# Performance work log

Measured on AMD Instinct MI355X. Metric: run time of the kernel, lower is better.

## Reference

```python
import jax, jax.numpy as jnp
import numpy as np

NODELEN = 394
N_NODES = 50000
N_EDGES = 200000
IN_DIM = 2 * NODELEN  # 788
H2 = 192
EMB = 128


def setup_inputs() -> dict:
    key = jax.random.key(0)
    ks = jax.random.split(key, 12)
    inp = {
        'features': jax.random.normal(ks[0], (N_NODES, NODELEN), dtype=jnp.float32),
        'src': jax.random.randint(ks[1], (N_EDGES,), 0, N_NODES),
        'dst': jax.random.randint(ks[2], (N_EDGES,), 0, N_NODES),
        # AutoEncoder params (Linear weights stored as [in, out])
        'W_enc1': jax.random.normal(ks[3], (IN_DIM, H2), dtype=jnp.float32) / np.sqrt(IN_DIM),
        'b_enc1': jnp.zeros((H2,), dtype=jnp.float32),
        'W_enc3': jax.random.normal(ks[4], (H2, EMB), dtype=jnp.float32) / np.sqrt(H2),
        'b_enc3': jnp.zeros((EMB,), dtype=jnp.float32),
        'W_dec1': jax.random.normal(ks[5], (EMB, H2), dtype=jnp.float32) / np.sqrt(EMB),
        'b_dec1': jnp.zeros((H2,), dtype=jnp.float32),
        'W_dec3': jax.random.normal(ks[6], (H2, IN_DIM), dtype=jnp.float32) / np.sqrt(H2),
        'b_dec3': jnp.zeros((IN_DIM,), dtype=jnp.float32),
    }
    return inp


def _segment_mean(msgs, dst, inv_deg, n):
    # msgs: [E, F] gathered neighbor features; mean over incoming edges per node
    return jax.ops.segment_sum(msgs, dst, num_segments=n) * inv_deg


def reference(features, src, dst, W_enc1, b_enc1, W_enc3, b_enc3,
              W_dec1, b_dec1, W_dec3, b_dec3):
    n = features.shape[0]
    ones = jnp.ones(src.shape[0], dtype=features.dtype)
    deg = jax.ops.segment_sum(ones, dst, num_segments=n)
    # nodes with no neighbors fall back to the zero dummy vector (as in source)
    inv_deg = (1.0 / jnp.maximum(deg, 1.0))[:, None]

    # depth-1 aggregation: mean of raw neighbor features, then feat[0] := 0
    h1 = _segment_mean(features[src], dst, inv_deg, n)
    h1 = h1.at[:, 0].set(0.0)
    # depth-2 aggregation: mean of depth-1 aggregates of neighbors, feat[0] := 0
    h2 = _segment_mean(h1[src], dst, inv_deg, n)
    h2 = h2.at[:, 0].set(0.0)

    # concatenated embedding with positions 0 and NODELEN zeroed
    emb = jnp.concatenate([features, h2], axis=1)  # [N, 788]
    emb = emb.at[:, 0].set(0.0).at[:, NODELEN].set(0.0)

    # AutoEncoder forward (dropout is identity at inference)
    x = jax.nn.relu(emb @ W_enc1 + b_enc1)
    encoded = x @ W_enc3 + b_enc3
    y = jax.nn.relu(encoded @ W_dec1 + b_dec1)
    decoded = y @ W_dec3 + b_dec3
    return encoded, decoded, emb
```

## Files before the change

### kernel.cpp

```cpp
#include <hip/hip_runtime.h>
#include <hip/hip_bf16.h>

#define NODELEN 394
#define IN_DIM 788
#define H2DIM 192
#define EMBDIM 128
#define NCHUNK 197

typedef __attribute__((ext_vector_type(4))) float f32x4;
typedef __attribute__((ext_vector_type(8))) short bfrag;

static __device__ __forceinline__ unsigned short f2bf(float f) {
    union { float f; unsigned u; } v; v.f = f;
    unsigned r = v.u + 0x7FFFu + ((v.u >> 16) & 1u);
    return (unsigned short)(r >> 16);
}
static __device__ __forceinline__ float bf2f(unsigned short h) {
    union { unsigned u; float f; } v; v.u = ((unsigned)h) << 16;
    return v.f;
}


__global__ void count_deg(const int* __restrict__ dst, int* __restrict__ deg, int e) {
    int i = blockIdx.x * blockDim.x + threadIdx.x;
    if (i < e) atomicAdd(&deg[dst[i]], 1);
}

__global__ void block_sum(const int* __restrict__ deg, int* __restrict__ bsum, int n) {
    __shared__ int s[256];
    int t = threadIdx.x;
    int i = blockIdx.x * 256 + t;
    s[t] = (i < n) ? deg[i] : 0;
    __syncthreads();
    for (int d = 128; d > 0; d >>= 1) {
        if (t < d) s[t] += s[t + d];
        __syncthreads();
    }
    if (t == 0) bsum[blockIdx.x] = s[0];
}

__global__ void scan_bsums(int* bsum, int nb) {
    __shared__ int s[256];
    int t = threadIdx.x;
    int x0 = (t < nb) ? bsum[t] : 0;
    s[t] = x0;
    __syncthreads();
    for (int d = 1; d < 256; d <<= 1) {
        int u = (t >= d) ? s[t - d] : 0;
        __syncthreads();
        s[t] += u;
        __syncthreads();
    }
    if (t < nb) bsum[t] = s[t] - x0;
}

__global__ void block_scan(const int* __restrict__ deg, const int* __restrict__ boff,
                           int* __restrict__ rowstart, int* __restrict__ cursor,
                           float* __restrict__ inv, int n) {
    __shared__ int s[256];
    int t = threadIdx.x;
    int i = blockIdx.x * 256 + t;
    int x0 = (i < n) ? deg[i] : 0;
    s[t] = x0;
    __syncthreads();
    for (int d = 1; d < 256; d <<= 1) {
        int u = (t >= d) ? s[t - d] : 0;
        __syncthreads();
        s[t] += u;
        __syncthreads();
    }
    if (i < n) {
        int r = boff[blockIdx.x] + s[t] - x0;
        rowstart[i] = r;
        cursor[i] = r;
        inv[i] = 1.0f / fmaxf((float)x0, 1.0f);
    }
}

__global__ void fill_edges(const int* __restrict__ src, const int* __restrict__ dst,
                           int* __restrict__ cursor, int* __restrict__ elist, int e) {
    int i = blockIdx.x * blockDim.x + threadIdx.x;
    if (i < e) {
        int p = atomicAdd(&cursor[dst[i]], 1);
        elist[p] = src[i];
    }
}


__global__ __launch_bounds__(256) void gather1(
        const float* __restrict__ feat, const int* __restrict__ rowstart,
        const int* __restrict__ deg, const float* __restrict__ inv,
        const int* __restrict__ elist, unsigned short* __restrict__ h1) {
    const int node = blockIdx.x;
    const int c = threadIdx.x;
    if (c >= NCHUNK) return;
    const int beg = rowstart[node];
    const int dc = deg[node];
    const float s = inv[node];
    const size_t off = (size_t)c * 2;

    float ax = 0.f, ay = 0.f, bx = 0.f, by = 0.f;
    float cx = 0.f, cy = 0.f, dx = 0.f, dy = 0.f;
    int j = 0;
    for (; j + 3 < dc; j += 4) {
        int n0 = elist[beg + j], n1 = elist[beg + j + 1];
        int n2 = elist[beg + j + 2], n3 = elist[beg + j + 3];
        float2 v0 = *(const float2*)(feat + (size_t)n0 * NODELEN + off);
        float2 v1 = *(const float2*)(feat + (size_t)n1 * NODELEN + off);
        float2 v2 = *(const float2*)(feat + (size_t)n2 * NODELEN + off);
        float2 v3 = *(const float2*)(feat + (size_t)n3 * NODELEN + off);
        ax += v0.x; ay += v0.y; bx += v1.x; by += v1.y;
        cx += v2.x; cy += v2.y; dx += v3.x; dy += v3.y;
    }
    for (; j < dc; ++j) {
        int n0 = elist[beg + j];
        float2 v0 = *(const float2*)(feat + (size_t)n0 * NODELEN + off);
        ax += v0.x; ay += v0.y;
    }
    float fx = (ax + bx + cx + dx) * s;
    float fy = (ay + by + cy + dy) * s;
    if (c == 0) fx = 0.f;
    unsigned out = ((unsigned)f2bf(fy) << 16) | (unsigned)f2bf(fx);
    *(unsigned*)(h1 + (size_t)node * NODELEN + off) = out;
}

__global__ __launch_bounds__(256) void gather2_emb(
        const float* __restrict__ feat, const unsigned* __restrict__ h1,
        const int* __restrict__ rowstart, const int* __restrict__ deg,
        const float* __restrict__ inv, const int* __restrict__ elist,
        float* __restrict__ emb, unsigned* __restrict__ emb16) {
    const int node = blockIdx.x;
    const int c = threadIdx.x;
    if (c >= NCHUNK) {
        if (emb16 && c >= NCHUNK && c < NCHUNK + 3) {
            int p = 394 + (c - NCHUNK) * 2;
            emb16[(size_t)node * 400 + p] = 0u;
            emb16[(size_t)node * 400 + p + 1] = 0u;
        }
        return;
    }
    const int beg = rowstart[node];
    const int dc = deg[node];
    const float s = inv[node];

    float ax = 0.f, ay = 0.f, bx = 0.f, by = 0.f;
    float cx = 0.f, cy = 0.f, dx = 0.f, dy = 0.f;
    int j = 0;
    for (; j + 3 < dc; j += 4) {
        int n0 = elist[beg + j], n1 = elist[beg + j + 1];
        int n2 = elist[beg + j + 2], n3 = elist[beg + j + 3];
        unsigned u0 = h1[(size_t)n0 * NCHUNK + c];
        unsigned u1 = h1[(size_t)n1 * NCHUNK + c];
        unsigned u2 = h1[(size_t)n2 * NCHUNK + c];
        unsigned u3 = h1[(size_t)n3 * NCHUNK + c];
        ax += bf2f((unsigned short)u0); ay += bf2f((unsigned short)(u0 >> 16));
        bx += bf2f((unsigned short)u1); by += bf2f((unsigned short)(u1 >> 16));
        cx += bf2f((unsigned short)u2); cy += bf2f((unsigned short)(u2 >> 16));
        dx += bf2f((unsigned short)u3); dy += bf2f((unsigned short)(u3 >> 16));
    }
    for (; j < dc; ++j) {
        int n0 = elist[beg + j];
        unsigned u0 = h1[(size_t)n0 * NCHUNK + c];
        ax += bf2f((unsigned short)u0); ay += bf2f((unsigned short)(u0 >> 16));
    }
    float hx = (ax + bx + cx + dx) * s;
    float hy = (ay + by + cy + dy) * s;

    const float* fr = feat + (size_t)node * NODELEN;
    float* er = emb + (size_t)node * IN_DIM;
    float2 fv = *(const float2*)(fr + c * 2);
    if (c == 0) { fv.x = 0.f; hx = 0.f; }
    *(float2*)(er + c * 2) = fv;
    float2 hv; hv.x = hx; hv.y = hy;
    *(float2*)(er + NODELEN + c * 2) = hv;

    if (emb16) {
        unsigned* e16 = emb16 + (size_t)node * 400;
        e16[c]          = ((unsigned)f2bf(fv.y) << 16) | (unsigned)f2bf(fv.x);
        e16[NCHUNK + c] = ((unsigned)f2bf(hy)  << 16) | (unsigned)f2bf(hx);
    }
}

__device__ __forceinline__ void tr_one(const float* W, unsigned short* Wt,
                                       int K, int N, int Kp, int idx) {
    int nrow = idx / Kp, k = idx - nrow * Kp;
    Wt[idx] = (k < K) ? f2bf(W[(size_t)k * N + nrow]) : (unsigned short)0;
}

#define T1E (192 * 800)
#define T2E (128 * 192)
#define T3E (192 * 128)
#define T4E (788 * 192)

__global__ void transpose_all(const float* __restrict__ W1, unsigned short* __restrict__ Wt1,
                              const float* __restrict__ W2, unsigned short* __restrict__ Wt2,
                              const float* __restrict__ W3, unsigned short* __restrict__ Wt3,
                              const float* __restrict__ W4, unsigned short* __restrict__ Wt4) {
    int idx = blockIdx.x * 256 + threadIdx.x;
    if (idx < T1E) { tr_one(W1, Wt1, IN_DIM, H2DIM, 800, idx); return; }
    idx -= T1E;
    if (idx < T2E) { tr_one(W2, Wt2, H2DIM, EMBDIM, 192, idx); return; }
    idx -= T2E;
    if (idx < T3E) { tr_one(W3, Wt3, EMBDIM, H2DIM, 128, idx); return; }
    idx -= T3E;
    if (idx < T4E) { tr_one(W4, Wt4, H2DIM, IN_DIM, 192, idx); return; }
}

template <int MF, int NF, int RELU, int A_F32, int OUTF, int OUTB>
__global__ __launch_bounds__(256) void gemm_mfma(
    const void* __restrict__ Aptr, const unsigned short* __restrict__ Wt,
    const float* __restrict__ bias, float* __restrict__ Cf,
    unsigned short* __restrict__ Cb, int M, int N, int K, int lda, int Ksteps)
{
    constexpr int BMr = 32 * MF;
    constexpr int BNr = 32 * NF;
    __shared__ unsigned short As[BMr][40];
    __shared__ unsigned short Bs[BNr][40];

    const int tid = threadIdx.x;
    const int wid = tid >> 6, l = tid & 63;
    const int wm = wid >> 1, wn = wid & 1;
    const int lr = l & 15, lk = l >> 4;
    const int m0 = blockIdx.x * BMr;
    const int n0 = blockIdx.y * BNr;
    const int Kp = Ksteps * 32;

    f32x4 acc[MF][NF];
    #pragma unroll
    for (int i = 0; i < MF; ++i)
        #pragma unroll
        for (int j = 0; j < NF; ++j)
            acc[i][j] = (f32x4){0.f, 0.f, 0.f, 0.f};

    float bv[NF];
    #pragma unroll
    for (int j = 0; j < NF; ++j) {
        int gn = n0 + wn * NF * 16 + j * 16 + lr;
        bv[j] = (gn < N) ? bias[gn] : 0.f;
    }

    for (int kt = 0; kt < Ksteps; ++kt) {
        int k0 = kt * 32;
        if (A_F32) {
            const float* A = (const float*)Aptr;
            for (int a = tid; a < BMr * 4; a += 256) {
                int row = a >> 2, q = a & 3;
                int gm = m0 + row, gk = k0 + q * 8;
                float4 v0 = make_float4(0.f, 0.f, 0.f, 0.f);
                float4 v1 = make_float4(0.f, 0.f, 0.f, 0.f);
                if (gm < M) {
                    if (gk < K)     v0 = *(const float4*)(A + (size_t)gm * lda + gk);
                    if (gk + 4 < K) v1 = *(const float4*)(A + (size_t)gm * lda + gk + 4);
                }
                union { unsigned short u[8]; bfrag v; } pk;
                pk.u[0] = f2bf(v0.x); pk.u[1] = f2bf(v0.y);
                pk.u[2] = f2bf(v0.z); pk.u[3] = f2bf(v0.w);
                pk.u[4] = f2bf(v1.x); pk.u[5] = f2bf(v1.y);
                pk.u[6] = f2bf(v1.z); pk.u[7] = f2bf(v1.w);
                *(bfrag*)&As[row][q * 8] = pk.v;
            }
        } else {
            const unsigned short* A = (const unsigned short*)Aptr;
            for (int a = tid; a < BMr * 2; a += 256) {
                int row = a >> 1, h = a & 1;
                int gm = m0 + row;
                bfrag v0 = {0,0,0,0,0,0,0,0}, v1 = {0,0,0,0,0,0,0,0};
                if (gm < M) {
                    const unsigned short* p = A + (size_t)gm * lda + k0 + h * 16;
                    v0 = *(const bfrag*)p;
                    v1 = *(const bfrag*)(p + 8);
                }
                *(bfrag*)&As[row][h * 16]     = v0;
                *(bfrag*)&As[row][h * 16 + 8] = v1;
            }
        }
        for (int a = tid; a < BNr * 2; a += 256) {
            int row = a >> 1, h = a & 1;
            int gn = n0 + row;
            bfrag v0 = {0,0,0,0,0,0,0,0}, v1 = {0,0,0,0,0,0,0,0};
            if (gn < N) {
                const unsigned short* p = Wt + (size_t)gn * Kp + k0 + h * 16;
                v0 = *(const bfrag*)p;
                v1 = *(const bfrag*)(p + 8);
            }
            *(bfrag*)&Bs[row][h * 16]     = v0;
            *(bfrag*)&Bs[row][h * 16 + 8] = v1;
        }
        __syncthreads();

        bfrag af[MF], bfr[NF];
        #pragma unroll
        for (int i = 0; i < MF; ++i)
            af[i] = *(const bfrag*)&As[wm * MF * 16 + i * 16 + lr][lk * 8];
        #pragma unroll
        for (int j = 0; j < NF; ++j)
            bfr[j] = *(const bfrag*)&Bs[wn * NF * 16 + j * 16 + lr][lk * 8];
        #pragma unroll
        for (int i = 0; i < MF; ++i)
            #pragma unroll
            for (int j = 0; j < NF; ++j)
                acc[i][j] = __builtin_amdgcn_mfma_f32_16x16x32_bf16(af[i], bfr[j], acc[i][j], 0, 0, 0);
        __syncthreads();
    }

    #pragma unroll
    for (int i = 0; i < MF; ++i) {
        #pragma unroll
        for (int j = 0; j < NF; ++j) {
            #pragma unroll
            for (int r = 0; r < 4; ++r) {
                int gm = m0 + wm * MF * 16 + i * 16 + lk * 4 + r;
                int gn = n0 + wn * NF * 16 + j * 16 + lr;
                if (gm < M && gn < N) {
                    float v = acc[i][j][r] + bv[j];
                    if (RELU) v = fmaxf(v, 0.f);
                    if (OUTF) Cf[(size_t)gm * N + gn] = v;
                    if (OUTB) Cb[(size_t)gm * N + gn] = f2bf(v);
                }
            }
        }
    }
}


extern "C" void kernel_launch(void* const* d_in, const int* in_sizes, int n_in,
                              void* d_out, int out_size, void* d_ws, size_t ws_size,
                              hipStream_t stream) {
    const float* features = (const float*)d_in[0];
    const int*   src      = (const int*)d_in[1];
    const int*   dst      = (const int*)d_in[2];
    const float* W_enc1   = (const float*)d_in[3];
    const float* b_enc1   = (const float*)d_in[4];
    const float* W_enc3   = (const float*)d_in[5];
    const float* b_enc3   = (const float*)d_in[6];
    const float* W_dec1   = (const float*)d_in[7];
    const float* b_dec1   = (const float*)d_in[8];
    const float* W_dec3   = (const float*)d_in[9];
    const float* b_dec3   = (const float*)d_in[10];

    const int n = in_sizes[0] / NODELEN;
    const int e = in_sizes[1];

    float* encoded = (float*)d_out;
    float* decoded = encoded + (size_t)n * EMBDIM;
    float* emb     = decoded + (size_t)n * IN_DIM;

    char* ws = (char*)d_ws;
    const size_t NEED_A = 134000000;
    const int useA = (ws_size >= NEED_A) ? 1 : 0;

    unsigned short* emb16;
    unsigned short* h1;
    unsigned short* x16, *enc16, *y16;
    unsigned short* Wt1, *Wt2, *Wt3, *Wt4;
    float* inv; int *deg, *rowstart, *cursor, *elist, *bsum;

    if (useA) {
        emb16    = (unsigned short*)(ws + 0);
        h1       = (unsigned short*)(ws + 80000000);
        x16      = (unsigned short*)(ws + 80000000);
        enc16    = (unsigned short*)(ws + 99200000);
        y16      = (unsigned short*)(ws + 112000000);
        Wt1      = (unsigned short*)(ws + 131200000);
        Wt2      = (unsigned short*)(ws + 131600000);
        Wt3      = (unsigned short*)(ws + 131700000);
        Wt4      = (unsigned short*)(ws + 131800000);
        inv      = (float*)(ws + 132200000);
        deg      = (int*)  (ws + 132400000);
        rowstart = (int*)  (ws + 132600000);
        cursor   = (int*)  (ws + 132800000);
        elist    = (int*)  (ws + 133000000);
        bsum     = (int*)  (ws + 133800000);
    } else {
        emb16    = nullptr;
        h1       = (unsigned short*)(ws + 0);
        x16      = (unsigned short*)(ws + 0);
        enc16    = (unsigned short*)(ws + 19200000);
        y16      = (unsigned short*)(ws + 32000000);
        Wt1      = (unsigned short*)(ws + 52000000);
        Wt2      = (unsigned short*)(ws + 52400000);
        Wt3      = (unsigned short*)(ws + 52500000);
        Wt4      = (unsigned short*)(ws + 52600000);
        inv      = (float*)(ws + 53000000);
        deg      = (int*)  (ws + 53200000);
        rowstart = (int*)  (ws + 53400000);
        cursor   = (int*)  (ws + 53600000);
        elist    = (int*)  (ws + 53800000);
        bsum     = (int*)  (ws + 54600000);
    }

    const int nb = (n + 255) / 256;
    const int eb = (e + 255) / 256;

    transpose_all<<<(T1E + T2E + T3E + T4E + 255) / 256, 256, 0, stream>>>(
        W_enc1, Wt1, W_enc3, Wt2, W_dec1, Wt3, W_dec3, Wt4);

    hipMemsetAsync(deg, 0, (size_t)n * sizeof(int), stream);
    count_deg<<<eb, 256, 0, stream>>>(dst, deg, e);
    block_sum<<<nb, 256, 0, stream>>>(deg, bsum, n);
    scan_bsums<<<1, 256, 0, stream>>>(bsum, nb);
    block_scan<<<nb, 256, 0, stream>>>(deg, bsum, rowstart, cursor, inv, n);
    fill_edges<<<eb, 256, 0, stream>>>(src, dst, cursor, elist, e);

    gather1<<<n, 256, 0, stream>>>(features, rowstart, deg, inv, elist, h1);
    gather2_emb<<<n, 256, 0, stream>>>(features, (const unsigned*)h1, rowstart, deg,
                                       inv, elist, emb, (unsigned*)emb16);

    const int MB = (n + 127) / 128;
    if (useA) {
        gemm_mfma<4, 6, 1, 0, 0, 1><<<dim3(MB, 1), 256, 0, stream>>>(
            emb16, Wt1, b_enc1, nullptr, x16, n, H2DIM, 800, 800, 25);
    } else {
        gemm_mfma<4, 6, 1, 1, 0, 1><<<dim3(MB, 1), 256, 0, stream>>>(
            emb, Wt1, b_enc1, nullptr, x16, n, H2DIM, IN_DIM, IN_DIM, 25);
    }
    gemm_mfma<4, 4, 0, 0, 1, 1><<<dim3(MB, 1), 256, 0, stream>>>(
        x16, Wt2, b_enc3, encoded, enc16, n, EMBDIM, H2DIM, H2DIM, 6);
    gemm_mfma<4, 6, 1, 0, 0, 1><<<dim3(MB, 1), 256, 0, stream>>>(
        enc16, Wt3, b_dec1, nullptr, y16, n, H2DIM, EMBDIM, EMBDIM, 4);
    gemm_mfma<4, 6, 0, 0, 1, 0><<<dim3(MB, 5), 256, 0, stream>>>(
        y16, Wt4, b_dec3, decoded, nullptr, n, IN_DIM, H2DIM, H2DIM, 6);
}
```

Baseline: 420.7 us.

## Fuse four autoencoder GEMMs into one kernel keeping intermediates in LDS

Replaces the four separate MFMA GEMM launches with a single kernel that processes 64-row tiles through encoder and decoder layers, holding hidden activations in shared memory instead of writing bf16 intermediates to global memory. It also drops the bf16 emb16 copy and reads the fp32 emb directly with conversion on load. This removes intermediate global traffic and three launches. In exchange it uses smaller M tiles with more weight reloads per block, serial per-block stages, and higher LDS usage that may limit occupancy.

Measured after the change: 387.7 us. 1.09x faster.

```diff
diff --git a/kernel.cpp b/kernel.cpp
--- a/kernel.cpp
+++ b/kernel.cpp
@@ -128,17 +128,10 @@
         const float* __restrict__ feat, const unsigned* __restrict__ h1,
         const int* __restrict__ rowstart, const int* __restrict__ deg,
         const float* __restrict__ inv, const int* __restrict__ elist,
-        float* __restrict__ emb, unsigned* __restrict__ emb16) {
+        float* __restrict__ emb) {
     const int node = blockIdx.x;
     const int c = threadIdx.x;
-    if (c >= NCHUNK) {
-        if (emb16 && c >= NCHUNK && c < NCHUNK + 3) {
-            int p = 394 + (c - NCHUNK) * 2;
-            emb16[(size_t)node * 400 + p] = 0u;
-            emb16[(size_t)node * 400 + p + 1] = 0u;
-        }
-        return;
-    }
+    if (c >= NCHUNK) return;
     const int beg = rowstart[node];
     const int dc = deg[node];
     const float s = inv[node];
@@ -173,12 +166,6 @@
     *(float2*)(er + c * 2) = fv;
     float2 hv; hv.x = hx; hv.y = hy;
     *(float2*)(er + NODELEN + c * 2) = hv;
-
-    if (emb16) {
-        unsigned* e16 = emb16 + (size_t)node * 400;
-        e16[c]          = ((unsigned)f2bf(fv.y) << 16) | (unsigned)f2bf(fv.x);
-        e16[NCHUNK + c] = ((unsigned)f2bf(hy)  << 16) | (unsigned)f2bf(hx);
-    }
 }
 
 __device__ __forceinline__ void tr_one(const float* W, unsigned short* Wt,
@@ -206,51 +193,44 @@
     if (idx < T4E) { tr_one(W4, Wt4, H2DIM, IN_DIM, 192, idx); return; }
 }
 
-template <int MF, int NF, int RELU, int A_F32, int OUTF, int OUTB>
-__global__ __launch_bounds__(256) void gemm_mfma(
-    const void* __restrict__ Aptr, const unsigned short* __restrict__ Wt,
-    const float* __restrict__ bias, float* __restrict__ Cf,
-    unsigned short* __restrict__ Cb, int M, int N, int K, int lda, int Ksteps)
+__global__ __launch_bounds__(256) void mlp_fused(
+    const float* __restrict__ emb,
+    const unsigned short* __restrict__ Wt1,
+    const unsigned short* __restrict__ Wt2,
+    const unsigned short* __restrict__ Wt3,
+    const unsigned short* __restrict__ Wt4,
+    const float* __restrict__ b1, const float* __restrict__ b2,
+    const float* __restrict__ b3, const float* __restrict__ b4,
+    float* __restrict__ encoded, float* __restrict__ decoded, int M)
 {
-    constexpr int BMr = 32 * MF;
-    constexpr int BNr = 32 * NF;
-    __shared__ unsigned short As[BMr][40];
-    __shared__ unsigned short Bs[BNr][40];
+    __shared__ unsigned short As[64][40];
+    __shared__ unsigned short Bs[192][40];
+    __shared__ unsigned short XY[64][200];
+    __shared__ unsigned short EN[64][136];
 
     const int tid = threadIdx.x;
     const int wid = tid >> 6, l = tid & 63;
     const int wm = wid >> 1, wn = wid & 1;
     const int lr = l & 15, lk = l >> 4;
-    const int m0 = blockIdx.x * BMr;
-    const int n0 = blockIdx.y * BNr;
-    const int Kp = Ksteps * 32;
-
-    f32x4 acc[MF][NF];
-    #pragma unroll
-    for (int i = 0; i < MF; ++i)
-        #pragma unroll
-        for (int j = 0; j < NF; ++j)
-            acc[i][j] = (f32x4){0.f, 0.f, 0.f, 0.f};
-
-    float bv[NF];
-    #pragma unroll
-    for (int j = 0; j < NF; ++j) {
-        int gn = n0 + wn * NF * 16 + j * 16 + lr;
-        bv[j] = (gn < N) ? bias[gn] : 0.f;
-    }
-
-    for (int kt = 0; kt < Ksteps; ++kt) {
-        int k0 = kt * 32;
-        if (A_F32) {
-            const float* A = (const float*)Aptr;
-            for (int a = tid; a < BMr * 4; a += 256) {
-                int row = a >> 2, q = a & 3;
+    const int m0 = blockIdx.x * 64;
+
+    {
+        f32x4 acc[2][6];
+        #pragma unroll
+        for (int i = 0; i < 2; ++i)
+            #pragma unroll
+            for (int j = 0; j < 6; ++j) acc[i][j] = (f32x4){0.f, 0.f, 0.f, 0.f};
+
+        for (int kt = 0; kt < 25; ++kt) {
+            const int k0 = kt * 32;
+            {
+                int row = tid >> 2, q = tid & 3;
                 int gm = m0 + row, gk = k0 + q * 8;
                 float4 v0 = make_float4(0.f, 0.f, 0.f, 0.f);
                 float4 v1 = make_float4(0.f, 0.f, 0.f, 0.f);
                 if (gm < M) {
-                    if (gk < K)     v0 = *(const float4*)(A + (size_t)gm * lda + gk);
-                    if (gk + 4 < K) v1 = *(const float4*)(A + (size_t)gm * lda + gk + 4);
+                    if (gk < IN_DIM)     v0 = *(const float4*)(emb + (size_t)gm * IN_DIM + gk);
+                    if (gk + 4 < IN_DIM) v1 = *(const float4*)(emb + (size_t)gm * IN_DIM + gk + 4);
                 }
                 union { unsigned short u[8]; bfrag v; } pk;
                 pk.u[0] = f2bf(v0.x); pk.u[1] = f2bf(v0.y);
@@ -259,66 +239,184 @@
                 pk.u[6] = f2bf(v1.z); pk.u[7] = f2bf(v1.w);
                 *(bfrag*)&As[row][q * 8] = pk.v;
             }
-        } else {
-            const unsigned short* A = (const unsigned short*)Aptr;
-            for (int a = tid; a < BMr * 2; a += 256) {
+            for (int a = tid; a < 384; a += 256) {
                 int row = a >> 1, h = a & 1;
-                int gm = m0 + row;
+                const unsigned short* p = Wt1 + (size_t)row * 800 + k0 + h * 16;
+                *(bfrag*)&Bs[row][h * 16]     = *(const bfrag*)p;
+                *(bfrag*)&Bs[row][h * 16 + 8] = *(const bfrag*)(p + 8);
+            }
+            __syncthreads();
+            bfrag af[2], bf[6];
+            #pragma unroll
+            for (int i = 0; i < 2; ++i) af[i] = *(const bfrag*)&As[wm * 32 + i * 16 + lr][lk * 8];
+            #pragma unroll
+            for (int j = 0; j < 6; ++j) bf[j] = *(const bfrag*)&Bs[wn * 96 + j * 16 + lr][lk * 8];
+            #pragma unroll
+            for (int i = 0; i < 2; ++i)
+                #pragma unroll
+                for (int j = 0; j < 6; ++j)
+                    acc[i][j] = __builtin_amdgcn_mfma_f32_16x16x32_bf16(af[i], bf[j], acc[i][j], 0, 0, 0);
+            __syncthreads();
+        }
+        float bv[6];
+        #pragma unroll
+        for (int j = 0; j < 6; ++j) bv[j] = b1[wn * 96 + j * 16 + lr];
+        #pragma unroll
+        for (int i = 0; i < 2; ++i)
+            #pragma unroll
+            for (int j = 0; j < 6; ++j)
+                #pragma unroll
+                for (int r = 0; r < 4; ++r) {
+                    int m = wm * 32 + i * 16 + lk * 4 + r;
+                    int n1 = wn * 96 + j * 16 + lr;
+                    XY[m][n1] = f2bf(fmaxf(acc[i][j][r] + bv[j], 0.f));
+                }
+        __syncthreads();
+    }
+
+    {
+        f32x4 acc[2][4];
+        #pragma unroll
+        for (int i = 0; i < 2; ++i)
+            #pragma unroll
+            for (int j = 0; j < 4; ++j) acc[i][j] = (f32x4){0.f, 0.f, 0.f, 0.f};
+
+        for (int kt = 0; kt < 6; ++kt) {
+            const int k0 = kt * 32;
+            {
+                int row = tid >> 1, h = tid & 1;
+                const unsigned short* p = Wt2 + (size_t)row * 192 + k0 + h * 16;
+                *(bfrag*)&Bs[row][h * 16]     = *(const bfrag*)p;
+                *(bfrag*)&Bs[row][h * 16 + 8] = *(const bfrag*)(p + 8);
+            }
+            __syncthreads();
+            bfrag af[2], bf[4];
+            #pragma unroll
+            for (int i = 0; i < 2; ++i) af[i] = *(const bfrag*)&XY[wm * 32 + i * 16 + lr][k0 + lk * 8];
+            #pragma unroll
+            for (int j = 0; j < 4; ++j) bf[j] = *(const bfrag*)&Bs[wn * 64 + j * 16 + lr][lk * 8];
+            #pragma unroll
+            for (int i = 0; i < 2; ++i)
+                #pragma unroll
+                for (int j = 0; j < 4; ++j)
+                    acc[i][j] = __builtin_amdgcn_mfma_f32_16x16x32_bf16(af[i], bf[j], acc[i][j], 0, 0, 0);
+            __syncthreads();
+        }
+        float bv[4];
+        #pragma unroll
+        for (int j = 0; j < 4; ++j) bv[j] = b2[wn * 64 + j * 16 + lr];
+        #pragma unroll
+        for (int i = 0; i < 2; ++i)
+            #pragma unroll
+            for (int j = 0; j < 4; ++j)
+                #pragma unroll
+                for (int r = 0; r < 4; ++r) {
+                    int m = wm * 32 + i * 16 + lk * 4 + r;
+                    int n2 = wn * 64 + j * 16 + lr;
+                    float v = acc[i][j][r] + bv[j];
+                    int gm = m0 + m;
+                    if (gm < M) encoded[(size_t)gm * EMBDIM + n2] = v;
+                    EN[m][n2] = f2bf(v);
+                }
+        __syncthreads();
+    }
+
+    {
+        f32x4 acc[2][6];
+        #pragma unroll
+        for (int i = 0; i < 2; ++i)
+            #pragma unroll
+            for (int j = 0; j < 6; ++j) acc[i][j] = (f32x4){0.f, 0.f, 0.f, 0.f};
+
+        for (int kt = 0; kt < 4; ++kt) {
+            const int k0 = kt * 32;
+            for (int a = tid; a < 384; a += 256) {
+                int row = a >> 1, h = a & 1;
+                const unsigned short* p = Wt3 + (size_t)row * 128 + k0 + h * 16;
+                *(bfrag*)&Bs[row][h * 16]     = *(const bfrag*)p;
+                *(bfrag*)&Bs[row][h * 16 + 8] = *(const bfrag*)(p + 8);
+            }
+            __syncthreads();
+            bfrag af[2], bf[6];
+            #pragma unroll
+            for (int i = 0; i < 2; ++i) af[i] = *(const bfrag*)&EN[wm * 32 + i * 16 + lr][k0 + lk * 8];
+            #pragma unroll
+            for (int j = 0; j < 6; ++j) bf[j] = *(const bfrag*)&Bs[wn * 96 + j * 16 + lr][lk * 8];
+            #pragma unroll
+            for (int i = 0; i < 2; ++i)
+                #pragma unroll
+                for (int j = 0; j < 6; ++j)
+                    acc[i][j] = __builtin_amdgcn_mfma_f32_16x16x32_bf16(af[i], bf[j], acc[i][j], 0, 0, 0);
+            __syncthreads();
+        }
+        float bv[6];
+        #pragma unroll
+        for (int j = 0; j < 6; ++j) bv[j] = b3[wn * 96 + j * 16 + lr];
+        #pragma unroll
+        for (int i = 0; i < 2; ++i)
+            #pragma unroll
+            for (int j = 0; j < 6; ++j)
+                #pragma unroll
+                for (int r = 0; r < 4; ++r) {
+                    int m = wm * 32 + i * 16 + lk * 4 + r;
+                    int n3 = wn * 96 + j * 16 + lr;
+                    XY[m][n3] = f2bf(fmaxf(acc[i][j][r] + bv[j], 0.f));
+                }
+        __syncthreads();
+    }
+
+    for (int nc = 0; nc < 7; ++nc) {
+        f32x4 acc[2][4];
+        #pragma unroll
+        for (int i = 0; i < 2; ++i)
+            #pragma unroll
+            for (int j = 0; j < 4; ++j) acc[i][j] = (f32x4){0.f, 0.f, 0.f, 0.f};
+
+        for (int kt = 0; kt < 6; ++kt) {
+            const int k0 = kt * 32;
+            {
+                int row = tid >> 1, h = tid & 1;
+                int gn = nc * 128 + row;
                 bfrag v0 = {0,0,0,0,0,0,0,0}, v1 = {0,0,0,0,0,0,0,0};
-                if (gm < M) {
-                    const unsigned short* p = A + (size_t)gm * lda + k0 + h * 16;
+                if (gn < IN_DIM) {
+                    const unsigned short* p = Wt4 + (size_t)gn * 192 + k0 + h * 16;
                     v0 = *(const bfrag*)p;
                     v1 = *(const bfrag*)(p + 8);
                 }
-                *(bfrag*)&As[row][h * 16]     = v0;
-                *(bfrag*)&As[row][h * 16 + 8] = v1;
+                *(bfrag*)&Bs[row][h * 16]     = v0;
+                *(bfrag*)&Bs[row][h * 16 + 8] = v1;
             }
+            __syncthreads();
+            bfrag af[2], bf[4];
+            #pragma unroll
+            for (int i = 0; i < 2; ++i) af[i] = *(const bfrag*)&XY[wm * 32 + i * 16 + lr][k0 + lk * 8];
+            #pragma unroll
+            for (int j = 0; j < 4; ++j) bf[j] = *(const bfrag*)&Bs[wn * 64 + j * 16 + lr][lk * 8];
+            #pragma unroll
+            for (int i = 0; i < 2; ++i)
+                #pragma unroll
+                for (int j = 0; j < 4; ++j)
+                    acc[i][j] = __builtin_amdgcn_mfma_f32_16x16x32_bf16(af[i], bf[j], acc[i][j], 0, 0, 0);
+            __syncthreads();
         }
-        for (int a = tid; a < BNr * 2; a += 256) {
-            int row = a >> 1, h = a & 1;
-            int gn = n0 + row;
-            bfrag v0 = {0,0,0,0,0,0,0,0}, v1 = {0,0,0,0,0,0,0,0};
-            if (gn < N) {
-                const unsigned short* p = Wt + (size_t)gn * Kp + k0 + h * 16;
-                v0 = *(const bfrag*)p;
-                v1 = *(const bfrag*)(p + 8);
-            }
-            *(bfrag*)&Bs[row][h * 16]     = v0;
-            *(bfrag*)&Bs[row][h * 16 + 8] = v1;
+        float bv[4];
+        #pragma unroll
+        for (int j = 0; j < 4; ++j) {
+            int n4 = nc * 128 + wn * 64 + j * 16 + lr;
+            bv[j] = (n4 < IN_DIM) ? b4[n4] : 0.f;
         }
-        __syncthreads();
-
-        bfrag af[MF], bfr[NF];
-        #pragma unroll
-        for (int i = 0; i < MF; ++i)
-            af[i] = *(const bfrag*)&As[wm * MF * 16 + i * 16 + lr][lk * 8];
-        #pragma unroll
-        for (int j = 0; j < NF; ++j)
-            bfr[j] = *(const bfrag*)&Bs[wn * NF * 16 + j * 16 + lr][lk * 8];
-        #pragma unroll
-        for (int i = 0; i < MF; ++i)
-            #pragma unroll
-            for (int j = 0; j < NF; ++j)
-                acc[i][j] = __builtin_amdgcn_mfma_f32_16x16x32_bf16(af[i], bfr[j], acc[i][j], 0, 0, 0);
-        __syncthreads();
-    }
-
-    #pragma unroll
-    for (int i = 0; i < MF; ++i) {
-        #pragma unroll
-        for (int j = 0; j < NF; ++j) {
-            #pragma unroll
-            for (int r = 0; r < 4; ++r) {
-                int gm = m0 + wm * MF * 16 + i * 16 + lk * 4 + r;
-                int gn = n0 + wn * NF * 16 + j * 16 + lr;
-                if (gm < M && gn < N) {
-                    float v = acc[i][j][r] + bv[j];
-                    if (RELU) v = fmaxf(v, 0.f);
-                    if (OUTF) Cf[(size_t)gm * N + gn] = v;
-                    if (OUTB) Cb[(size_t)gm * N + gn] = f2bf(v);
-                }
-            }
-        }
+        #pragma unroll
+        for (int i = 0; i < 2; ++i)
+            #pragma unroll
+            for (int j = 0; j < 4; ++j)
+                #pragma unroll
+                for (int r = 0; r < 4; ++r) {
+                    int m = wm * 32 + i * 16 + lk * 4 + r;
+                    int n4 = nc * 128 + wn * 64 + j * 16 + lr;
+                    int gm = m0 + m;
+                    if (gm < M && n4 < IN_DIM)
+                        decoded[(size_t)gm * IN_DIM + n4] = acc[i][j][r] + bv[j];
+                }
     }
 }
 
@@ -346,48 +444,17 @@
     float* emb     = decoded + (size_t)n * IN_DIM;
 
     char* ws = (char*)d_ws;
-    const size_t NEED_A = 134000000;
-    const int useA = (ws_size >= NEED_A) ? 1 : 0;
-
-    unsigned short* emb16;
-    unsigned short* h1;
-    unsigned short* x16, *enc16, *y16;
-    unsigned short* Wt1, *Wt2, *Wt3, *Wt4;
-    float* inv; int *deg, *rowstart, *cursor, *elist, *bsum;
-
-    if (useA) {
-        emb16    = (unsigned short*)(ws + 0);
-        h1       = (unsigned short*)(ws + 80000000);
-        x16      = (unsigned short*)(ws + 80000000);
-        enc16    = (unsigned short*)(ws + 99200000);
-        y16      = (unsigned short*)(ws + 112000000);
-        Wt1      = (unsigned short*)(ws + 131200000);
-        Wt2      = (unsigned short*)(ws + 131600000);
-        Wt3      = (unsigned short*)(ws + 131700000);
-        Wt4      = (unsigned short*)(ws + 131800000);
-        inv      = (float*)(ws + 132200000);
-        deg      = (int*)  (ws + 132400000);
-        rowstart = (int*)  (ws + 132600000);
-        cursor   = (int*)  (ws + 132800000);
-        elist    = (int*)  (ws + 133000000);
-        bsum     = (int*)  (ws + 133800000);
-    } else {
-        emb16    = nullptr;
-        h1       = (unsigned short*)(ws + 0);
-        x16      = (unsigned short*)(ws + 0);
-        enc16    = (unsigned short*)(ws + 19200000);
-        y16      = (unsigned short*)(ws + 32000000);
-        Wt1      = (unsigned short*)(ws + 52000000);
-        Wt2      = (unsigned short*)(ws + 52400000);
-        Wt3      = (unsigned short*)(ws + 52500000);
-        Wt4      = (unsigned short*)(ws + 52600000);
-        inv      = (float*)(ws + 53000000);
-        deg      = (int*)  (ws + 53200000);
-        rowstart = (int*)  (ws + 53400000);
-        cursor   = (int*)  (ws + 53600000);
-        elist    = (int*)  (ws + 53800000);
-        bsum     = (int*)  (ws + 54600000);
-    }
+    unsigned short* h1  = (unsigned short*)(ws + 0);
+    unsigned short* Wt1 = (unsigned short*)(ws + 40000000);
+    unsigned short* Wt2 = (unsigned short*)(ws + 40400000);
+    unsigned short* Wt3 = (unsigned short*)(ws + 40500000);
+    unsigned short* Wt4 = (unsigned short*)(ws + 40600000);
+    float* inv          = (float*)(ws + 41000000);
+    int*   deg          = (int*)  (ws + 41200000);
+    int*   rowstart     = (int*)  (ws + 41400000);
+    int*   cursor       = (int*)  (ws + 41600000);
+    int*   elist        = (int*)  (ws + 41800000);
+    int*   bsum         = (int*)  (ws + 42600000);
 
     const int nb = (n + 255) / 256;
     const int eb = (e + 255) / 256;
@@ -404,20 +471,10 @@
 
     gather1<<<n, 256, 0, stream>>>(features, rowstart, deg, inv, elist, h1);
     gather2_emb<<<n, 256, 0, stream>>>(features, (const unsigned*)h1, rowstart, deg,
-                                       inv, elist, emb, (unsigned*)emb16);
-
-    const int MB = (n + 127) / 128;
-    if (useA) {
-        gemm_mfma<4, 6, 1, 0, 0, 1><<<dim3(MB, 1), 256, 0, stream>>>(
-            emb16, Wt1, b_enc1, nullptr, x16, n, H2DIM, 800, 800, 25);
-    } else {
-        gemm_mfma<4, 6, 1, 1, 0, 1><<<dim3(MB, 1), 256, 0, stream>>>(
-            emb, Wt1, b_enc1, nullptr, x16, n, H2DIM, IN_DIM, IN_DIM, 25);
-    }
-    gemm_mfma<4, 4, 0, 0, 1, 1><<<dim3(MB, 1), 256, 0, stream>>>(
-        x16, Wt2, b_enc3, encoded, enc16, n, EMBDIM, H2DIM, H2DIM, 6);
-    gemm_mfma<4, 6, 1, 0, 0, 1><<<dim3(MB, 1), 256, 0, stream>>>(
-        enc16, Wt3, b_dec1, nullptr, y16, n, H2DIM, EMBDIM, EMBDIM, 4);
-    gemm_mfma<4, 6, 0, 0, 1, 0><<<dim3(MB, 5), 256, 0, stream>>>(
-        y16, Wt4, b_dec3, decoded, nullptr, n, IN_DIM, H2DIM, H2DIM, 6);
-}
+                                       inv, elist, emb);
+
+    const int MB = (n + 63) / 64;
+    mlp_fused<<<MB, 256, 0, stream>>>(emb, Wt1, Wt2, Wt3, Wt4,
+                                      b_enc1, b_enc3, b_dec1, b_dec3,
+                                      encoded, decoded, n);
+}
```
